# Optimization experiments

Hardware: AMD Instinct MI355X
Metric: run time of the kernel (lower is better)

## Reference

```python
import math
import jax, jax.numpy as jnp
import numpy as np

D_MODEL = 1024
N_STATE = 64
DT_MIN, DT_MAX = 1e-3, 1e-1
L_LEN = 2048


def setup_inputs() -> dict:
    key = jax.random.key(0)
    k_c, k_d, k_dt = jax.random.split(key, 3)
    n = jnp.arange(N_STATE, dtype=jnp.float32)
    A_real = -0.5 * jnp.ones((N_STATE,), dtype=jnp.float32)
    A_imag = math.pi * (n + 0.5)
    B = jnp.broadcast_to(jnp.sqrt(2.0 * n + 1.0)[:, None], (N_STATE, D_MODEL)).astype(jnp.float32)
    # C stored as real view (d_model, N, 2) like torch.view_as_real
    C = (jax.random.normal(k_c, (D_MODEL, N_STATE, 2), dtype=jnp.float32) * 0.5)
    D = jax.random.normal(k_d, (D_MODEL,), dtype=jnp.float32)
    log_dt = (jax.random.uniform(k_dt, (D_MODEL,), dtype=jnp.float32)
              * (math.log(DT_MAX) - math.log(DT_MIN)) + math.log(DT_MIN))
    return {"A_real": A_real, "A_imag": A_imag, "B": B, "C": C, "D": D,
            "log_dt": log_dt, "L": L_LEN}


def reference(A_real, A_imag, B, C, D, log_dt, L):
    dt = jnp.exp(log_dt)                              # (d,)
    A = A_real + 1j * A_imag                          # (N,) complex
    dtA = dt[:, None] * A[None, :]                    # (d, N)
    A_bar = (1.0 + dtA / 2.0) / (1.0 - dtA / 2.0)     # bilinear discretization
    B_bar = dt[:, None] * B.T / (1.0 - dtA / 2.0)     # (d, N)
    Cc = C[..., 0] + 1j * C[..., 1]                   # (d, N)
    ks = jnp.arange(L, dtype=jnp.float32)             # (L,)
    # Vandermonde powers: (d, N, L) complex — the big intermediate
    A_pow = A_bar[:, :, None] ** ks[None, None, :]
    K = jnp.real(jnp.sum((Cc * B_bar)[:, :, None] * A_pow, axis=1))  # (d, L)
    K = K.at[:, 0].add(D)                             # D * delta[0] skip term
    return K
```

## Files before the change

### kernel.cpp

```cpp
#include <hip/hip_runtime.h>
#include <math.h>

#define D_MODEL 1024
#define N_STATE 64
#define L_LEN   2048

__device__ __forceinline__ float eval_term(float lf,
                                           float th_hi, float th_lo, float ph0,
                                           float la_hi, float la_lo, float lw) {
    float amp = exp2f(fmaf(lf, la_hi, fmaf(lf, la_lo, lw)));
    float f1  = __builtin_amdgcn_fractf(lf * th_hi);
    float ph  = __builtin_amdgcn_fractf(f1 + fmaf(lf, th_lo, ph0));
    return amp * __builtin_amdgcn_cosf(ph);
}

__global__ __launch_bounds__(256) void s4d_kernel(
    const float* __restrict__ A_real, const float* __restrict__ A_imag,
    const float* __restrict__ B, const float* __restrict__ C,
    const float* __restrict__ Dv, const float* __restrict__ log_dt,
    float* __restrict__ out)
{
    __shared__ float s_th_hi[N_STATE], s_th_lo[N_STATE], s_ph[N_STATE];
    __shared__ float s_la_hi[N_STATE], s_la_lo[N_STATE], s_lw[N_STATE];
    __shared__ float s_ar[N_STATE], s_am[N_STATE];

    const int d = blockIdx.x;
    const int t = threadIdx.x;

    if (t < N_STATE) {
        const int n = t;
        const double dt = exp((double)log_dt[d]);
        const double zr = 0.5 * dt * (double)A_real[n];
        const double zi = 0.5 * dt * (double)A_imag[n];
        const double dr = 1.0 - zr, di = -zi;
        const double inv = 1.0 / (dr*dr + di*di);
        const double nr = 1.0 + zr, ni = zi;
        const double sr = (nr*dr + ni*di) * inv;
        const double si = (ni*dr - nr*di) * inv;
        const double dtB = dt * (double)B[n*D_MODEL + d];
        const double br = dtB * dr * inv;
        const double bi = dtB * zi * inv;
        const double cr = (double)C[(d*N_STATE + n)*2 + 0];
        const double ci = (double)C[(d*N_STATE + n)*2 + 1];
        const double wr = cr*br - ci*bi;
        const double wi = cr*bi + ci*br;

        const double INV2PI = 0.15915494309189535;
        const double threv = atan2(si, sr) * INV2PI;
        const double la    = 0.5 * log2(sr*sr + si*si);
        const double w2    = wr*wr + wi*wi;
        const double lw    = 0.5 * log2(fmax(w2, 1e-60));
        const double phrev = atan2(wi, wr) * INV2PI;

        const double th_hi = nearbyint(threv * 4096.0) * (1.0 / 4096.0);
        const double la_hi = nearbyint(la    * 4096.0) * (1.0 / 4096.0);
        s_th_hi[n] = (float)th_hi;
        s_th_lo[n] = (float)(threv - th_hi);
        s_la_hi[n] = (float)la_hi;
        s_la_lo[n] = (float)(la - la_hi);
        s_lw[n]    = (float)lw;
        s_ph[n]    = (float)phrev;

        double pr = sr, pq = si;
        #pragma unroll
        for (int k = 0; k < 4; ++k) {
            double a2 = pr*pr - pq*pq;
            double b2 = 2.0*pr*pq;
            pr = a2; pq = b2;
        }
        s_ar[n] = (float)(2.0 * pr);
        s_am[n] = (float)(pr*pr + pq*pq);
    }
    __syncthreads();

    const int wv   = t >> 6;
    const int lane = t & 63;
    const int q    = lane >> 4;
    const int g    = lane & 15;
    const int lbase = wv * 512 + g;
    const float dval = Dv[d];

    float y0[16], y1[16], ar[16], am[16];
    #pragma unroll
    for (int c = 0; c < 16; ++c) {
        const int n = (c << 2) | q;
        const float th_hi = s_th_hi[n], th_lo = s_th_lo[n], ph0 = s_ph[n];
        const float la_hi = s_la_hi[n], la_lo = s_la_lo[n], lw = s_lw[n];
        ar[c] = s_ar[n];
        am[c] = s_am[n];
        y0[c] = eval_term((float)lbase,        th_hi, th_lo, ph0, la_hi, la_lo, lw);
        y1[c] = eval_term((float)(lbase + 16), th_hi, th_lo, ph0, la_hi, la_lo, lw);
    }

    float* __restrict__ op = out + (size_t)d * L_LEN;

    #pragma unroll
    for (int i = 0; i < 32; ++i) {
        float r8[8];
        #pragma unroll
        for (int k = 0; k < 8; ++k) r8[k] = y0[2*k] + y0[2*k+1];
        float r4a = r8[0] + r8[1], r4b = r8[2] + r8[3];
        float r4c = r8[4] + r8[5], r4d = r8[6] + r8[7];
        float sum = (r4a + r4b) + (r4c + r4d);
        sum += __shfl_xor(sum, 16);
        sum += __shfl_xor(sum, 32);
        if (q == (i & 3)) {
            const int l = lbase + 16 * i;
            float v = sum;
            if (l == 0) v += dval;
            op[l] = v;
        }
        #pragma unroll
        for (int c = 0; c < 16; ++c) {
            float yn = fmaf(ar[c], y1[c], -(am[c] * y0[c]));
            y0[c] = y1[c];
            y1[c] = yn;
        }
    }
}

extern "C" void kernel_launch(void* const* d_in, const int* in_sizes, int n_in,
                              void* d_out, int out_size, void* d_ws, size_t ws_size,
                              hipStream_t stream) {
    const float* A_real = (const float*)d_in[0];
    const float* A_imag = (const float*)d_in[1];
    const float* B      = (const float*)d_in[2];
    const float* C      = (const float*)d_in[3];
    const float* Dv     = (const float*)d_in[4];
    const float* log_dt = (const float*)d_in[5];
    float* out = (float*)d_out;
    (void)in_sizes; (void)n_in; (void)d_ws; (void)ws_size; (void)out_size;

    s4d_kernel<<<dim3(D_MODEL), dim3(256), 0, stream>>>(
        A_real, A_imag, B, C, Dv, log_dt, out);
}
```

Before: 84.56 us.

## Split per-state double-precision setup into separate fully parallel kernel

Moves the fp64 per-(d,n) parameter computation (atan2, log2, complex division) out of the main kernel, where only 64 of 256 threads did it while the rest waited at a barrier, into a separate setup kernel that uses every thread. Parameters are written to workspace as packed float4s and read directly by the main kernel, which drops shared memory and the sync. This adds a second launch and a global-memory round trip of 2 MB of parameters.

Result: no change. 85.81 us (+1.5%).

```diff
diff --git a/kernel.cpp b/kernel.cpp
--- a/kernel.cpp
+++ b/kernel.cpp
@@ -4,6 +4,63 @@
 #define D_MODEL 1024
 #define N_STATE 64
 #define L_LEN   2048
+
+__global__ __launch_bounds__(256) void s4d_setup(
+    const float* __restrict__ A_real, const float* __restrict__ A_imag,
+    const float* __restrict__ B, const float* __restrict__ C,
+    const float* __restrict__ log_dt, float* __restrict__ par)
+{
+    const int id = blockIdx.x * 256 + threadIdx.x;
+    const int d = id >> 6;
+    const int n = id & 63;
+
+    const double dt = exp((double)log_dt[d]);
+    const double zr = 0.5 * dt * (double)A_real[n];
+    const double zi = 0.5 * dt * (double)A_imag[n];
+    const double dr = 1.0 - zr, di = -zi;
+    const double inv = 1.0 / (dr*dr + di*di);
+    const double nr = 1.0 + zr, ni = zi;
+    const double sr = (nr*dr + ni*di) * inv;
+    const double si = (ni*dr - nr*di) * inv;
+    const double dtB = dt * (double)B[n*D_MODEL + d];
+    const double br = dtB * dr * inv;
+    const double bi = dtB * zi * inv;
+    const double cr = (double)C[(d*N_STATE + n)*2 + 0];
+    const double ci = (double)C[(d*N_STATE + n)*2 + 1];
+    const double wr = cr*br - ci*bi;
+    const double wi = cr*bi + ci*br;
+
+    const double INV2PI = 0.15915494309189535;
+    const double threv = atan2(si, sr) * INV2PI;
+    const double la    = 0.5 * log2(sr*sr + si*si);
+    const double w2    = wr*wr + wi*wi;
+    const double lw    = 0.5 * log2(fmax(w2, 1e-60));
+    const double phrev = atan2(wi, wr) * INV2PI;
+
+    const double th_hi = nearbyint(threv * 4096.0) * (1.0 / 4096.0);
+    const double la_hi = nearbyint(la    * 4096.0) * (1.0 / 4096.0);
+
+    double pr = sr, pq = si;
+    #pragma unroll
+    for (int k = 0; k < 4; ++k) {
+        double a2 = pr*pr - pq*pq;
+        double b2 = 2.0*pr*pq;
+        pr = a2; pq = b2;
+    }
+
+    float4 p0, p1;
+    p0.x = (float)th_hi;
+    p0.y = (float)(threv - th_hi);
+    p0.z = (float)phrev;
+    p0.w = (float)la_hi;
+    p1.x = (float)(la - la_hi);
+    p1.y = (float)lw;
+    p1.z = (float)(2.0 * pr);
+    p1.w = (float)(pr*pr + pq*pq);
+    float4* o = (float4*)(par + (size_t)id * 8);
+    o[0] = p0;
+    o[1] = p1;
+}
 
 __device__ __forceinline__ float eval_term(float lf,
                                            float th_hi, float th_lo, float ph0,
@@ -14,84 +71,35 @@
     return amp * __builtin_amdgcn_cosf(ph);
 }
 
-__global__ __launch_bounds__(256) void s4d_kernel(
-    const float* __restrict__ A_real, const float* __restrict__ A_imag,
-    const float* __restrict__ B, const float* __restrict__ C,
-    const float* __restrict__ Dv, const float* __restrict__ log_dt,
+__global__ __launch_bounds__(256) void s4d_main(
+    const float* __restrict__ par, const float* __restrict__ Dv,
     float* __restrict__ out)
 {
-    __shared__ float s_th_hi[N_STATE], s_th_lo[N_STATE], s_ph[N_STATE];
-    __shared__ float s_la_hi[N_STATE], s_la_lo[N_STATE], s_lw[N_STATE];
-    __shared__ float s_ar[N_STATE], s_am[N_STATE];
-
     const int d = blockIdx.x;
     const int t = threadIdx.x;
-
-    if (t < N_STATE) {
-        const int n = t;
-        const double dt = exp((double)log_dt[d]);
-        const double zr = 0.5 * dt * (double)A_real[n];
-        const double zi = 0.5 * dt * (double)A_imag[n];
-        const double dr = 1.0 - zr, di = -zi;
-        const double inv = 1.0 / (dr*dr + di*di);
-        const double nr = 1.0 + zr, ni = zi;
-        const double sr = (nr*dr + ni*di) * inv;
-        const double si = (ni*dr - nr*di) * inv;
-        const double dtB = dt * (double)B[n*D_MODEL + d];
-        const double br = dtB * dr * inv;
-        const double bi = dtB * zi * inv;
-        const double cr = (double)C[(d*N_STATE + n)*2 + 0];
-        const double ci = (double)C[(d*N_STATE + n)*2 + 1];
-        const double wr = cr*br - ci*bi;
-        const double wi = cr*bi + ci*br;
-
-        const double INV2PI = 0.15915494309189535;
-        const double threv = atan2(si, sr) * INV2PI;
-        const double la    = 0.5 * log2(sr*sr + si*si);
-        const double w2    = wr*wr + wi*wi;
-        const double lw    = 0.5 * log2(fmax(w2, 1e-60));
-        const double phrev = atan2(wi, wr) * INV2PI;
-
-        const double th_hi = nearbyint(threv * 4096.0) * (1.0 / 4096.0);
-        const double la_hi = nearbyint(la    * 4096.0) * (1.0 / 4096.0);
-        s_th_hi[n] = (float)th_hi;
-        s_th_lo[n] = (float)(threv - th_hi);
-        s_la_hi[n] = (float)la_hi;
-        s_la_lo[n] = (float)(la - la_hi);
-        s_lw[n]    = (float)lw;
-        s_ph[n]    = (float)phrev;
-
-        double pr = sr, pq = si;
-        #pragma unroll
-        for (int k = 0; k < 4; ++k) {
-            double a2 = pr*pr - pq*pq;
-            double b2 = 2.0*pr*pq;
-            pr = a2; pq = b2;
-        }
-        s_ar[n] = (float)(2.0 * pr);
-        s_am[n] = (float)(pr*pr + pq*pq);
-    }
-    __syncthreads();
-
     const int wv   = t >> 6;
     const int lane = t & 63;
     const int q    = lane >> 4;
     const int g    = lane & 15;
     const int lbase = wv * 512 + g;
-    const float dval = Dv[d];
+
+    const float4* pp = (const float4*)(par + (size_t)d * (N_STATE * 8));
+    const float lf0 = (float)lbase;
+    const float lf1 = (float)(lbase + 16);
 
     float y0[16], y1[16], ar[16], am[16];
     #pragma unroll
     for (int c = 0; c < 16; ++c) {
         const int n = (c << 2) | q;
-        const float th_hi = s_th_hi[n], th_lo = s_th_lo[n], ph0 = s_ph[n];
-        const float la_hi = s_la_hi[n], la_lo = s_la_lo[n], lw = s_lw[n];
-        ar[c] = s_ar[n];
-        am[c] = s_am[n];
-        y0[c] = eval_term((float)lbase,        th_hi, th_lo, ph0, la_hi, la_lo, lw);
-        y1[c] = eval_term((float)(lbase + 16), th_hi, th_lo, ph0, la_hi, la_lo, lw);
+        const float4 a = pp[2*n];
+        const float4 b = pp[2*n + 1];
+        ar[c] = b.z;
+        am[c] = b.w;
+        y0[c] = eval_term(lf0, a.x, a.y, a.z, a.w, b.x, b.y);
+        y1[c] = eval_term(lf1, a.x, a.y, a.z, a.w, b.x, b.y);
     }
 
+    const float dval = Dv[d];
     float* __restrict__ op = out + (size_t)d * L_LEN;
 
     #pragma unroll
@@ -129,8 +137,10 @@
     const float* Dv     = (const float*)d_in[4];
     const float* log_dt = (const float*)d_in[5];
     float* out = (float*)d_out;
-    (void)in_sizes; (void)n_in; (void)d_ws; (void)ws_size; (void)out_size;
+    float* par = (float*)d_ws;
+    (void)in_sizes; (void)n_in; (void)ws_size; (void)out_size;
 
-    s4d_kernel<<<dim3(D_MODEL), dim3(256), 0, stream>>>(
-        A_real, A_imag, B, C, Dv, log_dt, out);
+    s4d_setup<<<dim3(D_MODEL * N_STATE / 256), dim3(256), 0, stream>>>(
+        A_real, A_imag, B, C, log_dt, par);
+    s4d_main<<<dim3(D_MODEL), dim3(256), 0, stream>>>(par, Dv, out);
 }
```
